# Optimization experiments

Hardware: AMD Instinct MI355X
Metric: run time of the kernel (lower is better)

The kernel has to match this reference:

```python
import jax, jax.numpy as jnp
import numpy as np

HIDDEN = 512
HEADS = 8
HEAD_DIM = HIDDEN // HEADS
INNER = int(HIDDEN * 4.0)
MAX_DIST = 512
LN_EPS = 1e-5


def _layernorm(x, g, b):
    mu = jnp.mean(x, axis=-1, keepdims=True)
    var = jnp.var(x, axis=-1, keepdims=True)
    return (x - mu) * jax.lax.rsqrt(var + LN_EPS) * g + b


def setup_inputs() -> dict:
    key = jax.random.key(0)
    ks = jax.random.split(key, 12)
    B, T = 4, 2048
    s = 0.02
    return {
        "x": jax.random.normal(ks[0], (B, T, HIDDEN), dtype=jnp.float32),
        "w_qkv": jax.random.normal(ks[1], (HIDDEN, 3 * HIDDEN), dtype=jnp.float32) * s,
        "b_qkv": jnp.zeros((3 * HIDDEN,), dtype=jnp.float32),
        "w_out": jax.random.normal(ks[2], (HIDDEN, HIDDEN), dtype=jnp.float32) * s,
        "b_out": jnp.zeros((HIDDEN,), dtype=jnp.float32),
        "ln1_g": jnp.ones((HIDDEN,), dtype=jnp.float32),
        "ln1_b": jnp.zeros((HIDDEN,), dtype=jnp.float32),
        "ln2_g": jnp.ones((HIDDEN,), dtype=jnp.float32),
        "ln2_b": jnp.zeros((HIDDEN,), dtype=jnp.float32),
        "w_mlp1": jax.random.normal(ks[3], (HIDDEN, INNER), dtype=jnp.float32) * s,
        "b_mlp1": jnp.zeros((INNER,), dtype=jnp.float32),
        "w_mlp2": jax.random.normal(ks[4], (INNER, HIDDEN), dtype=jnp.float32) * s,
        "b_mlp2": jnp.zeros((HIDDEN,), dtype=jnp.float32),
        "rel_table": jax.random.normal(ks[5], (2 * MAX_DIST + 1, HEADS), dtype=jnp.float32) * s,
    }


def reference(x, w_qkv, b_qkv, w_out, b_out, ln1_g, ln1_b, ln2_g, ln2_b,
              w_mlp1, b_mlp1, w_mlp2, b_mlp2, rel_table):
    B, T, C = x.shape
    scale = HEAD_DIM ** -0.5
    qkv = x @ w_qkv + b_qkv  # [B,T,3C]
    qkv = qkv.reshape(B, T, 3, HEADS, HEAD_DIM)
    q = qkv[:, :, 0].transpose(0, 2, 1, 3)  # [B,H,T,D]
    k = qkv[:, :, 1].transpose(0, 2, 1, 3)
    v = qkv[:, :, 2].transpose(0, 2, 1, 3)
    logits = jnp.einsum('bhqd,bhkd->bhqk', q, k) * scale
    # relative position bias: clamp(q_pos - k_pos) lookup -> [H,T,T]
    rel = jnp.clip(jnp.arange(T)[:, None] - jnp.arange(T)[None, :], -MAX_DIST, MAX_DIST) + MAX_DIST
    bias = rel_table[rel].transpose(2, 0, 1)  # [H,T,T]
    logits = logits + bias[None]
    attn = jax.nn.softmax(logits, axis=-1)
    out = jnp.einsum('bhqk,bhkd->bhqd', attn, v)
    out = out.transpose(0, 2, 1, 3).reshape(B, T, C)
    out = out @ w_out + b_out
    x = _layernorm(x + out, ln1_g, ln1_b)
    h = jax.nn.gelu(x @ w_mlp1 + b_mlp1, approximate=False)
    mlp_out = h @ w_mlp2 + b_mlp2
    return _layernorm(x + mlp_out, ln2_g, ln2_b)
```

## Files before the change

### kernel.cpp

```cpp
#include <hip/hip_runtime.h>
#include <hip/hip_bf16.h>

using bf16 = __hip_bfloat16;
typedef __attribute__((ext_vector_type(8))) short bf16x8;
typedef __attribute__((ext_vector_type(4))) short bf16x4;
typedef __attribute__((ext_vector_type(4))) float f32x4;

#define HIDDEN 512
#define HEADS 8
#define HDIM 64
#define INNER 2048
#define MAXD 512
#define BB 4
#define TT 2048
#define MM (BB*TT)
#define LOG2E 1.44269504088896340736f

typedef const __attribute__((address_space(1))) unsigned int* gas_u32p;
typedef __attribute__((address_space(3))) unsigned int* las_u32p;

__device__ __forceinline__ void gload_lds16(const void* g, void* l) {
    __builtin_amdgcn_global_load_lds((gas_u32p)g, (las_u32p)l, 16, 0, 0);
}
__device__ __forceinline__ short bfr(float x) {
    return (short)__bfloat16_as_ushort(__float2bfloat16(x));
}

__global__ __launch_bounds__(256) void cast_kernel(const float* __restrict__ in,
                                                   bf16* __restrict__ out) {
    int i = (blockIdx.x * 256 + threadIdx.x) * 4;
    float4 v = *(const float4*)&in[i];
    bf16 o[4] = {__float2bfloat16(v.x), __float2bfloat16(v.y),
                 __float2bfloat16(v.z), __float2bfloat16(v.w)};
    *(bf16x4*)&out[i] = *(bf16x4*)o;
}

__global__ __launch_bounds__(256) void wtrans_kernel(const float* __restrict__ in,
                                                     bf16* __restrict__ out,
                                                     int K, int N) {
    __shared__ float tile[32][33];
    int bx = blockIdx.x;
    int by = blockIdx.y;
    int lx = threadIdx.x & 31, ly = threadIdx.x >> 5;
    #pragma unroll
    for (int i = 0; i < 4; ++i)
        tile[ly + 8*i][lx] = in[(size_t)(by*32 + ly + 8*i) * N + bx*32 + lx];
    __syncthreads();
    #pragma unroll
    for (int i = 0; i < 4; ++i)
        out[(size_t)(bx*32 + ly + 8*i) * K + by*32 + lx] =
            __float2bfloat16(tile[lx][ly + 8*i]);
}

template<int EPI, int BN, int VT, int RESID>
__global__ __launch_bounds__(256) void gemm_kernel(
    const bf16* __restrict__ A, const bf16* __restrict__ BT,
    const float* __restrict__ bias, const float* __restrict__ resid,
    void* __restrict__ C, bf16* __restrict__ vt_out,
    int M, int N, int K)
{
    constexpr int NBF = BN / 32;
    constexpr int BBYTES = BN * 64;
    __shared__ __align__(16) bf16 As[3*128*32];
    __shared__ __align__(16) bf16 Bs[3*BN*32];
    const int tid = threadIdx.x;
    const int wid = tid >> 6;
    const int lane = tid & 63;
    const int lhi = lane >> 4, llo = lane & 15;
    const int m0 = blockIdx.x * 128, n0 = blockIdx.y * BN;
    const int wr = wid >> 1, wc = wid & 1;

    const int srow = tid >> 2, scol = (tid & 3) * 8;
    const bf16* Ap = A + (size_t)(m0 + srow) * K + scol;
    const bf16* Bp = BT + (size_t)(n0 + srow) * K + scol;
    const size_t step64 = (size_t)64 * K;

    f32x4 acc[4][NBF] = {};

    auto STAGE = [&](int t, int bi) {
        const int k = t << 5;
        gload_lds16(Ap + k,          (char*)As + bi*8192 + tid*16);
        gload_lds16(Ap + k + step64, (char*)As + bi*8192 + 4096 + tid*16);
        gload_lds16(Bp + k,          (char*)Bs + bi*BBYTES + tid*16);
        if (BN == 128) gload_lds16(Bp + k + step64, (char*)Bs + bi*BBYTES + 4096 + tid*16);
    };

    const int NK = K >> 5;
    STAGE(0, 0);
    STAGE(1, 1);
    if constexpr (BN == 128) asm volatile("s_waitcnt vmcnt(4)" ::: "memory");
    else                     asm volatile("s_waitcnt vmcnt(3)" ::: "memory");
    __builtin_amdgcn_s_barrier();
    __builtin_amdgcn_sched_barrier(0);

    int p = 0;
    for (int it = 0; it < NK; ++it) {
        const int pn2 = (p == 0) ? 2 : p - 1;
        if (it + 2 < NK) STAGE(it + 2, pn2);
        bf16x8 af[4], bfrg[NBF];
        #pragma unroll
        for (int ar = 0; ar < 4; ++ar)
            af[ar] = *(const bf16x8*)((const char*)As + p*8192 + (64*wr + 16*ar + llo)*64 + lhi*16);
        #pragma unroll
        for (int bc = 0; bc < NBF; ++bc)
            bfrg[bc] = *(const bf16x8*)((const char*)Bs + p*BBYTES + ((BN/2)*wc + 16*bc + llo)*64 + lhi*16);
        #pragma unroll
        for (int ar = 0; ar < 4; ++ar)
            #pragma unroll
            for (int bc = 0; bc < NBF; ++bc)
                acc[ar][bc] = __builtin_amdgcn_mfma_f32_16x16x32_bf16(
                    af[ar], bfrg[bc], acc[ar][bc], 0, 0, 0);
        if constexpr (BN == 128) asm volatile("s_waitcnt vmcnt(4)" ::: "memory");
        else                     asm volatile("s_waitcnt vmcnt(3)" ::: "memory");
        __builtin_amdgcn_s_barrier();
        __builtin_amdgcn_sched_barrier(0);
        p = (p == 2) ? 0 : p + 1;
    }

    if (VT && n0 >= 1024) {
        #pragma unroll
        for (int ar = 0; ar < 4; ++ar) {
            const int row = m0 + 64*wr + 16*ar + 4*lhi;
            const int bq = row >> 11, t0 = row & 2047;
            #pragma unroll
            for (int bc = 0; bc < NBF; ++bc) {
                const int cv = n0 - 1024 + (BN/2)*wc + 16*bc + llo;
                const int h = cv >> 6, d = cv & 63;
                float bv = bias[n0 + (BN/2)*wc + 16*bc + llo];
                bf16x4 pk = {bfr(acc[ar][bc][0] + bv), bfr(acc[ar][bc][1] + bv),
                             bfr(acc[ar][bc][2] + bv), bfr(acc[ar][bc][3] + bv)};
                *(bf16x4*)&vt_out[(((size_t)(bq*8 + h) * 64 + d) << 11) + t0] = pk;
            }
        }
        return;
    }

    #pragma unroll
    for (int ar = 0; ar < 4; ++ar) {
        #pragma unroll
        for (int j = 0; j < 4; ++j) {
            int row = m0 + 64*wr + 16*ar + 4*lhi + j;
            #pragma unroll
            for (int bc = 0; bc < NBF; ++bc) {
                int col = n0 + (BN/2)*wc + 16*bc + llo;
                float v = acc[ar][bc][j] + bias[col];
                if (RESID) v += resid[(size_t)row * N + col];
                if (EPI == 2) {
                    float u = 0.7978845608028654f * (v + 0.044715f * v * v * v);
                    float e = __builtin_amdgcn_exp2f(u * (2.0f * LOG2E));
                    v = v * (1.0f - 1.0f / (1.0f + e));
                }
                if (EPI == 1)
                    ((float*)C)[(size_t)row * N + col] = v;
                else
                    ((bf16*)C)[(size_t)row * N + col] = __float2bfloat16(v);
            }
        }
    }
}

#define PTN (TT + 128)
__global__ __launch_bounds__(512) void attn_kernel(
    const bf16* __restrict__ qkv,
    const bf16* __restrict__ v_t,
    const float* __restrict__ rel_table,
    bf16* __restrict__ attn_out)
{
    __shared__ __align__(16) bf16 Ks[3*64*64];
    __shared__ __align__(16) bf16 Vs[3*64*64];
    __shared__ __align__(16) bf16 Ps[8][16*64];
    __shared__ float PT[PTN];

    const int qt = blockIdx.x, bh = blockIdx.y;
    const int b = bh >> 3, h = bh & 7;
    const int tid = threadIdx.x, wid = tid >> 6, lane = tid & 63;
    const int lhi = lane >> 4, llo = lane & 15;

    const int lo = qt * 128 - (TT - 1);
    for (int i = tid; i < PTN; i += 512) {
        int idx = min(max(i + lo, -MAXD), MAXD) + MAXD;
        PT[i] = rel_table[(size_t)idx * HEADS + h] * LOG2E;
    }

    const int q0w = qt * 128 + wid * 16;
    const int q = q0w + llo;
    bf16x8 bq[2];
    #pragma unroll
    for (int kc = 0; kc < 2; ++kc)
        bq[kc] = *(const bf16x8*)&qkv[(size_t)(b*TT + q) * 1536 + h*64 + kc*32 + lhi*8];

    const int so = tid * 16;
    const int r0 = so >> 7;
    const int c0 = (((so & 127) ^ ((r0 & 7) << 4)) >> 1);
    const bf16* kbase = qkv + (size_t)(b*TT) * 1536 + 512 + h*64;
    const bf16* vbase = v_t + (size_t)bh * 64 * TT;

    float accL = 0.f;
    f32x4 accO[4] = {};
    const int pti = wid*16 + llo + (TT - 1);

    auto STAGE = [&](int t, int bi) {
        const int kv = t * 64;
        gload_lds16(kbase + (size_t)(kv + r0) * 1536 + c0, (char*)Ks + bi*8192 + so);
        gload_lds16(vbase + (size_t)r0 * TT + kv + c0,     (char*)Vs + bi*8192 + so);
    };

    constexpr int NT = TT / 64;
    STAGE(0, 0);
    STAGE(1, 1);
    asm volatile("s_waitcnt vmcnt(2) lgkmcnt(0)" ::: "memory");
    __builtin_amdgcn_s_barrier();
    __builtin_amdgcn_sched_barrier(0);

    int p = 0;
    for (int kt = 0; kt < NT; ++kt) {
        const int kv0 = kt * 64;
        const int pn2 = (p == 0) ? 2 : p - 1;
        if (kt + 2 < NT) STAGE(kt + 2, pn2);
        const char* Kb = (const char*)Ks + p*8192;
        const char* Vb = (const char*)Vs + p*8192;

        f32x4 s[4];
        __builtin_amdgcn_s_setprio(1);
        #pragma unroll
        for (int f = 0; f < 4; ++f) {
            f32x4 a = {};
            const int rr = 16*f + llo;
            #pragma unroll
            for (int kc = 0; kc < 2; ++kc) {
                bf16x8 ak = *(const bf16x8*)(Kb + rr*128 + (((4*kc + lhi) ^ (rr & 7)) << 4));
                a = __builtin_amdgcn_mfma_f32_16x16x32_bf16(ak, bq[kc], a, 0, 0, 0);
            }
            s[f] = a;
        }
        __builtin_amdgcn_s_setprio(0);

        const int ib = pti - kv0;
        #pragma unroll
        for (int f = 0; f < 4; ++f)
            #pragma unroll
            for (int j = 0; j < 4; ++j)
                s[f][j] = s[f][j] * (0.125f * LOG2E) + PT[ib - 16*f - 4*lhi - j];
        float tf[4];
        #pragma unroll
        for (int f = 0; f < 4; ++f) {
            float p0 = __builtin_amdgcn_exp2f(s[f][0]);
            float p1 = __builtin_amdgcn_exp2f(s[f][1]);
            float p2 = __builtin_amdgcn_exp2f(s[f][2]);
            float p3 = __builtin_amdgcn_exp2f(s[f][3]);
            tf[f] = (p0 + p1) + (p2 + p3);
            bf16x4 pk = {bfr(p0), bfr(p1), bfr(p2), bfr(p3)};
            *(bf16x4*)((char*)Ps + wid*2048 + llo*128 +
                       ((f*32 + lhi*8) ^ ((llo & 7) << 4))) = pk;
        }
        accL += (tf[0] + tf[1]) + (tf[2] + tf[3]);

        bf16x8 pf[2];
        #pragma unroll
        for (int kc = 0; kc < 2; ++kc)
            pf[kc] = *(const bf16x8*)((const char*)Ps + wid*2048 + llo*128 +
                                      ((kc*64 + lhi*16) ^ ((llo & 7) << 4)));
        __builtin_amdgcn_s_setprio(1);
        #pragma unroll
        for (int kc = 0; kc < 2; ++kc)
            #pragma unroll
            for (int f = 0; f < 4; ++f) {
                const int rr = 16*f + llo;
                bf16x8 av = *(const bf16x8*)(Vb + rr*128 + (((4*kc + lhi) ^ (rr & 7)) << 4));
                accO[f] = __builtin_amdgcn_mfma_f32_16x16x32_bf16(av, pf[kc], accO[f], 0, 0, 0);
            }
        __builtin_amdgcn_s_setprio(0);

        asm volatile("s_waitcnt vmcnt(2)" ::: "memory");
        __builtin_amdgcn_s_barrier();
        __builtin_amdgcn_sched_barrier(0);
        p = (p == 2) ? 0 : p + 1;
    }

    accL += __shfl_xor(accL, 16, 64);
    accL += __shfl_xor(accL, 32, 64);
    const float rl = 1.0f / accL;
    const int row = b*TT + q;
    #pragma unroll
    for (int f = 0; f < 4; ++f) {
        bf16x4 ov = {bfr(accO[f][0] * rl), bfr(accO[f][1] * rl),
                     bfr(accO[f][2] * rl), bfr(accO[f][3] * rl)};
        *(bf16x4*)&attn_out[(size_t)row * HIDDEN + h*64 + 16*f + 4*lhi] = ov;
    }
}

template<int WB>
__global__ __launch_bounds__(256) void ln_kernel(
    const float* __restrict__ in,
    const float* __restrict__ g, const float* __restrict__ bb,
    float* __restrict__ of, bf16* __restrict__ ob)
{
    int row = blockIdx.x * 4 + (threadIdx.x >> 6);
    int lane = threadIdx.x & 63;
    const float* pa = in + (size_t)row * HIDDEN;
    float v[8];
    float s = 0.f, sq = 0.f;
    #pragma unroll
    for (int i = 0; i < 2; ++i) {
        float4 a4 = *(const float4*)&pa[lane*4 + i*256];
        v[i*4+0] = a4.x; v[i*4+1] = a4.y; v[i*4+2] = a4.z; v[i*4+3] = a4.w;
        #pragma unroll
        for (int j = 0; j < 4; ++j) { s += v[i*4+j]; sq += v[i*4+j]*v[i*4+j]; }
    }
    #pragma unroll
    for (int d = 1; d < 64; d <<= 1) {
        s  += __shfl_xor(s,  d, 64);
        sq += __shfl_xor(sq, d, 64);
    }
    float mean = s * (1.f / HIDDEN);
    float var  = sq * (1.f / HIDDEN) - mean * mean;
    float rstd = rsqrtf(var + 1e-5f);
    #pragma unroll
    for (int i = 0; i < 2; ++i)
        #pragma unroll
        for (int j = 0; j < 4; ++j) {
            int col = lane*4 + i*256 + j;
            float o = (v[i*4+j] - mean) * rstd * g[col] + bb[col];
            of[(size_t)row * HIDDEN + col] = o;
            if (WB) ob[(size_t)row * HIDDEN + col] = __float2bfloat16(o);
        }
}

extern "C" void kernel_launch(void* const* d_in, const int* in_sizes, int n_in,
                              void* d_out, int out_size, void* d_ws, size_t ws_size,
                              hipStream_t stream) {
    const float* x     = (const float*)d_in[0];
    const float* w_qkv = (const float*)d_in[1];
    const float* b_qkv = (const float*)d_in[2];
    const float* w_out = (const float*)d_in[3];
    const float* b_out = (const float*)d_in[4];
    const float* ln1_g = (const float*)d_in[5];
    const float* ln1_b = (const float*)d_in[6];
    const float* ln2_g = (const float*)d_in[7];
    const float* ln2_b = (const float*)d_in[8];
    const float* w1    = (const float*)d_in[9];
    const float* b1    = (const float*)d_in[10];
    const float* w2    = (const float*)d_in[11];
    const float* b2    = (const float*)d_in[12];
    const float* rel   = (const float*)d_in[13];
    float* out = (float*)d_out;

    char* ws = (char*)d_ws;
    bf16*  xb     = (bf16*)(ws + 0);
    bf16*  wqkv_t = (bf16*)(ws + 8388608);
    bf16*  wout_t = (bf16*)(ws + 9961472);
    bf16*  w1_t   = (bf16*)(ws + 10485760);
    bf16*  w2_t   = (bf16*)(ws + 12582912);
    bf16*  qkv    = (bf16*)(ws + 14680064);
    bf16*  v_t    = (bf16*)(ws + 39845888);
    bf16*  attn_o = (bf16*)(ws + 48234496);
    float* proj   = (float*)(ws + 56623104);
    float* x1     = (float*)(ws + 73400320);
    bf16*  h      = (bf16*)(ws + 14680064);
    bf16*  x1b    = (bf16*)(ws + 90177536);

    cast_kernel<<<MM*HIDDEN/4/256, 256, 0, stream>>>(x, xb);
    wtrans_kernel<<<dim3(1536/32, 512/32),  256, 0, stream>>>(w_qkv, wqkv_t, 512, 1536);
    wtrans_kernel<<<dim3(512/32,  512/32),  256, 0, stream>>>(w_out, wout_t, 512, 512);
    wtrans_kernel<<<dim3(2048/32, 512/32),  256, 0, stream>>>(w1,    w1_t,   512, 2048);
    wtrans_kernel<<<dim3(512/32,  2048/32), 256, 0, stream>>>(w2,    w2_t,   2048, 512);
    gemm_kernel<0,128,1,0><<<dim3(MM/128, 1536/128), 256, 0, stream>>>(
        xb, wqkv_t, b_qkv, nullptr, qkv, v_t, MM, 1536, 512);
    attn_kernel<<<dim3(TT/128, BB*HEADS), 512, 0, stream>>>(qkv, v_t, rel, attn_o);
    gemm_kernel<1,64,0,1><<<dim3(MM/128, 512/64), 256, 0, stream>>>(
        attn_o, wout_t, b_out, x, proj, nullptr, MM, 512, 512);
    ln_kernel<1><<<MM/4, 256, 0, stream>>>(proj, ln1_g, ln1_b, x1, x1b);
    gemm_kernel<2,128,0,0><<<dim3(MM/128, 2048/128), 256, 0, stream>>>(
        x1b, w1_t, b1, nullptr, h, nullptr, MM, 2048, 512);
    gemm_kernel<1,64,0,1><<<dim3(MM/128, 512/64), 256, 0, stream>>>(
        h, w2_t, b2, x1, proj, nullptr, MM, 512, 2048);
    ln_kernel<0><<<MM/4, 256, 0, stream>>>(proj, ln2_g, ln2_b, out, nullptr);
}
```

Before: 196.3 us.

## Give each attention wave two query sub-tiles to reuse K/V fragments

The attention kernel now uses 4 waves of 256 threads per block, each handling 32 query rows (two 16-row sub-tiles) instead of 8 waves each with 16 rows. Each K and V fragment read from LDS feeds two MFMAs, halving LDS read traffic per MFMA. Each thread now issues two global-to-LDS loads per tensor per stage, and the wait counts are adjusted to match. The trade-off is more registers per wave (doubled accumulators) and fewer waves per block to hide latency.

```diff
diff --git a/kernel.cpp b/kernel.cpp
--- a/kernel.cpp
+++ b/kernel.cpp
@@ -160,7 +160,7 @@
 }
 
 #define PTN (TT + 128)
-__global__ __launch_bounds__(512) void attn_kernel(
+__global__ __launch_bounds__(256) void attn_kernel(
     const bf16* __restrict__ qkv,
     const bf16* __restrict__ v_t,
     const float* __restrict__ rel_table,
@@ -168,7 +168,7 @@
 {
     __shared__ __align__(16) bf16 Ks[3*64*64];
     __shared__ __align__(16) bf16 Vs[3*64*64];
-    __shared__ __align__(16) bf16 Ps[8][16*64];
+    __shared__ __align__(16) bf16 Ps[4*32*64];
     __shared__ float PT[PTN];
 
     const int qt = blockIdx.x, bh = blockIdx.y;
@@ -177,17 +177,19 @@
     const int lhi = lane >> 4, llo = lane & 15;
 
     const int lo = qt * 128 - (TT - 1);
-    for (int i = tid; i < PTN; i += 512) {
+    for (int i = tid; i < PTN; i += 256) {
         int idx = min(max(i + lo, -MAXD), MAXD) + MAXD;
         PT[i] = rel_table[(size_t)idx * HEADS + h] * LOG2E;
     }
 
-    const int q0w = qt * 128 + wid * 16;
-    const int q = q0w + llo;
-    bf16x8 bq[2];
-    #pragma unroll
-    for (int kc = 0; kc < 2; ++kc)
-        bq[kc] = *(const bf16x8*)&qkv[(size_t)(b*TT + q) * 1536 + h*64 + kc*32 + lhi*8];
+    const int q0w = qt * 128 + wid * 32;
+    bf16x8 bq[2][2];
+    #pragma unroll
+    for (int qh = 0; qh < 2; ++qh)
+        #pragma unroll
+        for (int kc = 0; kc < 2; ++kc)
+            bq[qh][kc] = *(const bf16x8*)&qkv[(size_t)(b*TT + q0w + 16*qh + llo) * 1536
+                                              + h*64 + kc*32 + lhi*8];
 
     const int so = tid * 16;
     const int r0 = so >> 7;
@@ -195,20 +197,21 @@
     const bf16* kbase = qkv + (size_t)(b*TT) * 1536 + 512 + h*64;
     const bf16* vbase = v_t + (size_t)bh * 64 * TT;
 
-    float accL = 0.f;
-    f32x4 accO[4] = {};
-    const int pti = wid*16 + llo + (TT - 1);
+    float accL[2] = {};
+    f32x4 accO[2][4] = {};
 
     auto STAGE = [&](int t, int bi) {
         const int kv = t * 64;
-        gload_lds16(kbase + (size_t)(kv + r0) * 1536 + c0, (char*)Ks + bi*8192 + so);
-        gload_lds16(vbase + (size_t)r0 * TT + kv + c0,     (char*)Vs + bi*8192 + so);
+        gload_lds16(kbase + (size_t)(kv + r0) * 1536 + c0,      (char*)Ks + bi*8192 + so);
+        gload_lds16(kbase + (size_t)(kv + r0 + 32) * 1536 + c0, (char*)Ks + bi*8192 + so + 4096);
+        gload_lds16(vbase + (size_t)r0 * TT + kv + c0,          (char*)Vs + bi*8192 + so);
+        gload_lds16(vbase + (size_t)(r0 + 32) * TT + kv + c0,   (char*)Vs + bi*8192 + so + 4096);
     };
 
     constexpr int NT = TT / 64;
     STAGE(0, 0);
     STAGE(1, 1);
-    asm volatile("s_waitcnt vmcnt(2) lgkmcnt(0)" ::: "memory");
+    asm volatile("s_waitcnt vmcnt(4) lgkmcnt(0)" ::: "memory");
     __builtin_amdgcn_s_barrier();
     __builtin_amdgcn_sched_barrier(0);
 
@@ -220,72 +223,87 @@
         const char* Kb = (const char*)Ks + p*8192;
         const char* Vb = (const char*)Vs + p*8192;
 
-        f32x4 s[4];
+        f32x4 s[2][4] = {};
         __builtin_amdgcn_s_setprio(1);
         #pragma unroll
         for (int f = 0; f < 4; ++f) {
-            f32x4 a = {};
             const int rr = 16*f + llo;
             #pragma unroll
             for (int kc = 0; kc < 2; ++kc) {
                 bf16x8 ak = *(const bf16x8*)(Kb + rr*128 + (((4*kc + lhi) ^ (rr & 7)) << 4));
-                a = __builtin_amdgcn_mfma_f32_16x16x32_bf16(ak, bq[kc], a, 0, 0, 0);
-            }
-            s[f] = a;
+                #pragma unroll
+                for (int qh = 0; qh < 2; ++qh)
+                    s[qh][f] = __builtin_amdgcn_mfma_f32_16x16x32_bf16(
+                        ak, bq[qh][kc], s[qh][f], 0, 0, 0);
+            }
         }
         __builtin_amdgcn_s_setprio(0);
 
-        const int ib = pti - kv0;
-        #pragma unroll
-        for (int f = 0; f < 4; ++f)
-            #pragma unroll
-            for (int j = 0; j < 4; ++j)
-                s[f][j] = s[f][j] * (0.125f * LOG2E) + PT[ib - 16*f - 4*lhi - j];
-        float tf[4];
+        #pragma unroll
+        for (int qh = 0; qh < 2; ++qh) {
+            const int ibq = wid*32 + 16*qh + llo + (TT - 1) - kv0 - 4*lhi;
+            #pragma unroll
+            for (int f = 0; f < 4; ++f)
+                #pragma unroll
+                for (int j = 0; j < 4; ++j)
+                    s[qh][f][j] = s[qh][f][j] * (0.125f * LOG2E) + PT[ibq - 16*f - j];
+            float tf[4];
+            const int prow = qt ? 0 : 0;
+            #pragma unroll
+            for (int f = 0; f < 4; ++f) {
+                float p0 = __builtin_amdgcn_exp2f(s[qh][f][0]);
+                float p1 = __builtin_amdgcn_exp2f(s[qh][f][1]);
+                float p2 = __builtin_amdgcn_exp2f(s[qh][f][2]);
+                float p3 = __builtin_amdgcn_exp2f(s[qh][f][3]);
+                tf[f] = (p0 + p1) + (p2 + p3);
+                bf16x4 pk = {bfr(p0), bfr(p1), bfr(p2), bfr(p3)};
+                *(bf16x4*)((char*)Ps + wid*4096 + (16*qh + llo)*128 +
+                           ((f*32 + lhi*8) ^ ((llo & 7) << 4))) = pk;
+            }
+            accL[qh] += (tf[0] + tf[1]) + (tf[2] + tf[3]);
+        }
+
+        bf16x8 pf[2][2];
+        #pragma unroll
+        for (int qh = 0; qh < 2; ++qh)
+            #pragma unroll
+            for (int kc = 0; kc < 2; ++kc)
+                pf[qh][kc] = *(const bf16x8*)((const char*)Ps + wid*4096 + (16*qh + llo)*128 +
+                                              ((kc*64 + lhi*16) ^ ((llo & 7) << 4)));
+        __builtin_amdgcn_s_setprio(1);
         #pragma unroll
         for (int f = 0; f < 4; ++f) {
-            float p0 = __builtin_amdgcn_exp2f(s[f][0]);
-            float p1 = __builtin_amdgcn_exp2f(s[f][1]);
-            float p2 = __builtin_amdgcn_exp2f(s[f][2]);
-            float p3 = __builtin_amdgcn_exp2f(s[f][3]);
-            tf[f] = (p0 + p1) + (p2 + p3);
-            bf16x4 pk = {bfr(p0), bfr(p1), bfr(p2), bfr(p3)};
-            *(bf16x4*)((char*)Ps + wid*2048 + llo*128 +
-                       ((f*32 + lhi*8) ^ ((llo & 7) << 4))) = pk;
-        }
-        accL += (tf[0] + tf[1]) + (tf[2] + tf[3]);
-
-        bf16x8 pf[2];
-        #pragma unroll
-        for (int kc = 0; kc < 2; ++kc)
-            pf[kc] = *(const bf16x8*)((const char*)Ps + wid*2048 + llo*128 +
-                                      ((kc*64 + lhi*16) ^ ((llo & 7) << 4)));
-        __builtin_amdgcn_s_setprio(1);
-        #pragma unroll
-        for (int kc = 0; kc < 2; ++kc)
-            #pragma unroll
-            for (int f = 0; f < 4; ++f) {
-                const int rr = 16*f + llo;
+            const int rr = 16*f + llo;
+            #pragma unroll
+            for (int kc = 0; kc < 2; ++kc) {
                 bf16x8 av = *(const bf16x8*)(Vb + rr*128 + (((4*kc + lhi) ^ (rr & 7)) << 4));
-                accO[f] = __builtin_amdgcn_mfma_f32_16x16x32_bf16(av, pf[kc], accO[f], 0, 0, 0);
-            }
+                #pragma unroll
+                for (int qh = 0; qh < 2; ++qh)
+                    accO[qh][f] = __builtin_amdgcn_mfma_f32_16x16x32_bf16(
+                        av, pf[qh][kc], accO[qh][f], 0, 0, 0);
+            }
+        }
         __builtin_amdgcn_s_setprio(0);
 
-        asm volatile("s_waitcnt vmcnt(2)" ::: "memory");
+        asm volatile("s_waitcnt vmcnt(4)" ::: "memory");
         __builtin_amdgcn_s_barrier();
         __builtin_amdgcn_sched_barrier(0);
         p = (p == 2) ? 0 : p + 1;
     }
 
-    accL += __shfl_xor(accL, 16, 64);
-    accL += __shfl_xor(accL, 32, 64);
-    const float rl = 1.0f / accL;
-    const int row = b*TT + q;
-    #pragma unroll
-    for (int f = 0; f < 4; ++f) {
-        bf16x4 ov = {bfr(accO[f][0] * rl), bfr(accO[f][1] * rl),
-                     bfr(accO[f][2] * rl), bfr(accO[f][3] * rl)};
-        *(bf16x4*)&attn_out[(size_t)row * HIDDEN + h*64 + 16*f + 4*lhi] = ov;
+    #pragma unroll
+    for (int qh = 0; qh < 2; ++qh) {
+        float l = accL[qh];
+        l += __shfl_xor(l, 16, 64);
+        l += __shfl_xor(l, 32, 64);
+        const float rl = 1.0f / l;
+        const int row = b*TT + q0w + 16*qh + llo;
+        #pragma unroll
+        for (int f = 0; f < 4; ++f) {
+            bf16x4 ov = {bfr(accO[qh][f][0] * rl), bfr(accO[qh][f][1] * rl),
+                         bfr(accO[qh][f][2] * rl), bfr(accO[qh][f][3] * rl)};
+            *(bf16x4*)&attn_out[(size_t)row * HIDDEN + h*64 + 16*f + 4*lhi] = ov;
+        }
     }
 }
 
@@ -366,7 +384,7 @@
     wtrans_kernel<<<dim3(512/32,  2048/32), 256, 0, stream>>>(w2,    w2_t,   2048, 512);
     gemm_kernel<0,128,1,0><<<dim3(MM/128, 1536/128), 256, 0, stream>>>(
         xb, wqkv_t, b_qkv, nullptr, qkv, v_t, MM, 1536, 512);
-    attn_kernel<<<dim3(TT/128, BB*HEADS), 512, 0, stream>>>(qkv, v_t, rel, attn_o);
+    attn_kernel<<<dim3(TT/128, BB*HEADS), 256, 0, stream>>>(qkv, v_t, rel, attn_o);
     gemm_kernel<1,64,0,1><<<dim3(MM/128, 512/64), 256, 0, stream>>>(
         attn_o, wout_t, b_out, x, proj, nullptr, MM, 512, 512);
     ln_kernel<1><<<MM/4, 256, 0, stream>>>(proj, ln1_g, ln1_b, x1, x1b);
```

After: 205.0 us. +4.4%, slower.
